# Optimization experiments

Measured on AMD Instinct MI355X. Metric: run time of the kernel, lower is better.

Reference implementation:

```python
import jax, jax.numpy as jnp
import numpy as np
from jax.scipy.special import logsumexp

S, D, K, R, P = 500, 768, 16, 256, 64  # seq_len, bert_dim, out_dim, n_pairs, max wordpieces/entity


def setup_inputs() -> dict:
    key = jax.random.key(0)
    k1, k2, k3, k4, k5, k6 = jax.random.split(key, 6)
    word_embeddings = jax.random.normal(k1, (S, D), jnp.float32)
    # kaiming_normal_ fan_in = D*K (last two dims collapsed); gain sqrt(2) for relu
    W = jax.random.normal(k2, (D, K, D), jnp.float32) * np.float32((2.0 / (K * D)) ** 0.5)
    idx1 = jax.random.randint(k3, (R, P), 0, S)
    idx2 = jax.random.randint(k4, (R, P), 0, S)
    # ragged mention lengths -> padding masks (at least 1 valid wordpiece)
    len1 = jax.random.randint(k5, (R,), 1, P + 1)
    len2 = jax.random.randint(k6, (R,), 1, P + 1)
    pos = jnp.arange(P)
    mask1 = (pos[None, :] < len1[:, None]).astype(jnp.float32)
    mask2 = (pos[None, :] < len2[:, None]).astype(jnp.float32)
    return {"word_embeddings": word_embeddings, "W": W, "idx1": idx1, "idx2": idx2,
            "mask1": mask1, "mask2": mask2}


def reference(word_embeddings, W, idx1, idx2, mask1, mask2):
    # gather ragged mention wordpieces (padded to P per entity)
    e1 = word_embeddings[idx1]  # [R, P, D]
    e2 = word_embeddings[idx2]  # [R, P, D]
    # biaffine: z[r,k,p,q] = e1[r,p,:] @ W[:,k,:] @ e2[r,q,:]
    zh = jnp.einsum('rpd,dke->rpke', e1, W)      # [R, P, K, D]
    z = jnp.einsum('rpke,rqe->rkpq', zh, e2)     # [R, K, P, P]
    # logsumexp pooling over all valid (p, q) mention-token pairs
    b = mask1[:, None, :, None] * mask2[:, None, None, :]  # [R, 1, P, P]
    scores = logsumexp(z, axis=(2, 3), b=b)      # [R, K]
    return scores
```

## Files before the change

kernel.cpp:

```cpp
#include <hip/hip_runtime.h>
#include <math.h>

#define S_ 500
#define D_ 768
#define K_ 16
#define R_ 256
#define P_ 64
#define NT 12

typedef unsigned short ushort_t;
typedef __attribute__((ext_vector_type(8))) short short8;
typedef __attribute__((ext_vector_type(4))) float floatx4;
typedef __attribute__((ext_vector_type(4))) float fx4;

__device__ inline ushort_t f2bf(float x) {
  unsigned int u = __float_as_uint(x);
  u += 0x7fffu + ((u >> 16) & 1u);
  return (ushort_t)(u >> 16);
}

__device__ inline unsigned int cvtpk(float lo, float hi) {
  unsigned int r;
  asm("v_cvt_pk_bf16_f32 %0, %1, %2" : "=v"(r) : "v"(lo), "v"(hi));
  return r;
}

#define GLD_LDS16(g, l)                                                        \
  __builtin_amdgcn_global_load_lds(                                            \
      (const __attribute__((address_space(1))) void*)(g),                      \
      (__attribute__((address_space(3))) void*)(l), 16, 0, 0)

#define ASM_BARRIER asm volatile("s_barrier" ::: "memory")
#define WAIT_VM6 asm volatile("s_waitcnt vmcnt(6)" ::: "memory")
#define WAIT_VM0 asm volatile("s_waitcnt vmcnt(0)" ::: "memory")

#define CFENCE asm volatile("" ::: "memory")
#define BARRIER_SYNC                                                           \
  do { CFENCE; __builtin_amdgcn_s_barrier(); CFENCE; } while (0)
#define WAIT_VM20_F                                                            \
  do { asm volatile("s_waitcnt vmcnt(20)" ::: "memory");                       \
       __builtin_amdgcn_sched_barrier(0); } while (0)
#define WAIT_VM0_F                                                             \
  do { asm volatile("s_waitcnt vmcnt(0)" ::: "memory");                        \
       __builtin_amdgcn_sched_barrier(0); } while (0)
#define WAIT_LGKM0_F                                                           \
  do { asm volatile("s_waitcnt lgkmcnt(0)" ::: "memory");                      \
       __builtin_amdgcn_sched_barrier(0); } while (0)

__global__ __launch_bounds__(256) void prep(const float* __restrict__ WE,
                                            ushort_t* __restrict__ WEb) {
  const int t = threadIdx.x;
  int gid = blockIdx.x * 256 + t;
  int row = gid / 192;
  ushort4 o = {0, 0, 0, 0};
  if (row < S_) {
    float4 v = *(const float4*)(WE + (size_t)gid * 4);
    o.x = f2bf(v.x); o.y = f2bf(v.y); o.z = f2bf(v.z); o.w = f2bf(v.w);
  }
  *(ushort4*)(WEb + (size_t)gid * 4) = o;
}

__global__ __launch_bounds__(256, 2) void mm0_fused(const ushort_t* __restrict__ A,
                                                    const float* __restrict__ Wf,
                                                    ushort_t* __restrict__ C) {
  __shared__ ushort_t As[2][2][128 * 32];
  __shared__ ushort_t Bs[2][2][128 * 32];
  const int tid = threadIdx.x;
  const int wave = tid >> 6, lane = tid & 63;
  const int m0 = blockIdx.y * 128, n0 = blockIdx.x * 128;
  const int wm = (wave & 1) * 64, wn = (wave >> 1) * 64;
  const int col = lane & 15, quad = lane >> 4;

  floatx4 acc[4][4];
#pragma unroll
  for (int i = 0; i < 4; i++)
#pragma unroll
    for (int j = 0; j < 4; j++)
#pragma unroll
      for (int e = 0; e < 4; e++) acc[i][j][e] = 0.f;

  const int srow = wave * 32 + (lane >> 2);
  const int scol = (lane & 3) * 8;
  const ushort_t* ga0 = A + (size_t)(m0 + srow) * D_ + scol;
  const int ldsbase = (wave * 32) * 32;

#define ISSUE_A(t_, buf_)                                                      \
  do {                                                                         \
    const ushort_t* ga = ga0 + (t_)*64;                                        \
    GLD_LDS16(ga, &As[buf_][0][ldsbase]);                                      \
    GLD_LDS16(ga + 16 * D_, &As[buf_][0][ldsbase + 16 * 32]);                  \
    GLD_LDS16(ga + 32, &As[buf_][1][ldsbase]);                                 \
    GLD_LDS16(ga + 32 + 16 * D_, &As[buf_][1][ldsbase + 16 * 32]);             \
  } while (0)

  const int nq = tid & 31;
  const int dqA = tid >> 5;
  const float* gwA = Wf + (size_t)(dqA * 4) * 12288 + n0 + nq * 4;
  const float* gwB = gwA + (size_t)32 * 12288;

  fx4 bv[2][4];
#define LOADB(t_)                                                              \
  do {                                                                         \
    _Pragma("unroll") for (int i = 0; i < 4; i++) {                            \
      bv[0][i] = *(const fx4*)(gwA + (size_t)((t_)*64 + i) * 12288);           \
      bv[1][i] = *(const fx4*)(gwB + (size_t)((t_)*64 + i) * 12288);           \
    }                                                                          \
  } while (0)

#define WRITEB(buf_)                                                           \
  do {                                                                         \
    _Pragma("unroll") for (int h = 0; h < 2; h++)                              \
    _Pragma("unroll") for (int j = 0; j < 4; j++) {                            \
      int row = nq * 4 + j;                                                    \
      uint2 w;                                                                 \
      w.x = cvtpk(bv[h][0][j], bv[h][1][j]);                                   \
      w.y = cvtpk(bv[h][2][j], bv[h][3][j]);                                   \
      *(uint2*)((char*)&Bs[buf_][h][0] +                                       \
                ((row * 64 + dqA * 8) ^ ((nq & 15) << 4))) = w;                \
    }                                                                          \
  } while (0)

  LOADB(0);
  ISSUE_A(0, 0);
  WRITEB(0);
  WAIT_LGKM0_F;
  for (int t = 0; t < NT; ++t) {
    const int cur = t & 1;
    if (t + 1 < NT) {
      LOADB(t + 1);
      ISSUE_A(t + 1, cur ^ 1);
      WAIT_VM20_F;
    } else {
      WAIT_VM0_F;
    }
    BARRIER_SYNC;
#pragma unroll
    for (int s = 0; s < 2; ++s) {
      short8 a[4], b[4];
#pragma unroll
      for (int i = 0; i < 4; i++)
        a[i] = *(const short8*)&As[cur][s][(wm + i * 16 + col) * 32 + quad * 8];
#pragma unroll
      for (int j = 0; j < 4; j++) {
        int row = wn + j * 16 + col;
        b[j] = *(const short8*)((const char*)&Bs[cur][s][0] +
                                ((row * 64 + quad * 16) ^ (((row >> 2) & 15) << 4)));
      }
#pragma unroll
      for (int i = 0; i < 4; i++)
#pragma unroll
        for (int j = 0; j < 4; j++)
          acc[i][j] = __builtin_amdgcn_mfma_f32_16x16x32_bf16(b[j], a[i], acc[i][j], 0, 0, 0);
    }
    if (t + 1 < NT) {
      WRITEB(cur ^ 1);
      WAIT_LGKM0_F;
    }
    BARRIER_SYNC;
  }
#undef ISSUE_A
#undef LOADB
#undef WRITEB

#pragma unroll
  for (int i = 0; i < 4; i++) {
    int m = m0 + wm + i * 16 + col;
#pragma unroll
    for (int j = 0; j < 4; j++) {
      int n = n0 + wn + j * 16 + quad * 4;
      ushort4 o;
      o.x = f2bf(acc[i][j][0]); o.y = f2bf(acc[i][j][1]);
      o.z = f2bf(acc[i][j][2]); o.w = f2bf(acc[i][j][3]);
      *(ushort4*)(C + (size_t)m * 12288 + n) = o;
    }
  }
}

__global__ __launch_bounds__(256, 2) void mm1_bt(const ushort_t* __restrict__ A,
                                                 const ushort_t* __restrict__ Bm,
                                                 ushort_t* __restrict__ G) {
  __shared__ ushort_t As[2][2][128 * 32];
  __shared__ ushort_t Bs[2][2][64 * 32];
  const int tid = threadIdx.x;
  const int wave = tid >> 6, lane = tid & 63;
  const int lin = blockIdx.x + (blockIdx.y << 3);
  const int yb = ((lin & 7) << 3) | (lin >> 6);
  const int xb = (lin >> 3) & 7;
  const int m0 = yb * 128, n0 = xb * 64;
  const int wm = (wave & 1) * 64, wn = (wave >> 1) * 32;
  const int col = lane & 15, quad = lane >> 4;

  floatx4 acc[4][2];
#pragma unroll
  for (int i = 0; i < 4; i++)
#pragma unroll
    for (int j = 0; j < 2; j++)
#pragma unroll
      for (int e = 0; e < 4; e++) acc[i][j][e] = 0.f;

  const int lrow = lane >> 2, scol = (lane & 3) * 8;
  const ushort_t* ga0 = A + (size_t)(m0 + wave * 32 + lrow) * D_ + scol;
  const ushort_t* gb0 = Bm + (size_t)(n0 + wave * 16 + lrow) * D_ + scol;
  const int aoff = (wave * 32) * 32;
  const int boff = (wave * 16) * 32;

#define ISSUE_TILE1(t_, buf_)                                                  \
  do {                                                                         \
    _Pragma("unroll") for (int s_ = 0; s_ < 2; s_++) {                         \
      const ushort_t* ga = ga0 + (t_)*64 + s_ * 32;                            \
      const ushort_t* gb = gb0 + (t_)*64 + s_ * 32;                            \
      GLD_LDS16(ga, &As[buf_][s_][aoff]);                                      \
      GLD_LDS16(ga + 16 * D_, &As[buf_][s_][aoff + 16 * 32]);                  \
      GLD_LDS16(gb, &Bs[buf_][s_][boff]);                                      \
    }                                                                          \
  } while (0)

  ISSUE_TILE1(0, 0);
  for (int t = 0; t < NT; ++t) {
    const int cur = t & 1;
    if (t + 1 < NT) {
      ISSUE_TILE1(t + 1, cur ^ 1);
      WAIT_VM6;
    } else {
      WAIT_VM0;
    }
    ASM_BARRIER;
#pragma unroll
    for (int s = 0; s < 2; ++s) {
      short8 a[4], b[2];
#pragma unroll
      for (int i = 0; i < 4; i++)
        a[i] = *(const short8*)&As[cur][s][(wm + i * 16 + col) * 32 + quad * 8];
#pragma unroll
      for (int j = 0; j < 2; j++)
        b[j] = *(const short8*)&Bs[cur][s][(wn + j * 16 + col) * 32 + quad * 8];
#pragma unroll
      for (int i = 0; i < 4; i++)
#pragma unroll
        for (int j = 0; j < 2; j++)
          acc[i][j] = __builtin_amdgcn_mfma_f32_16x16x32_bf16(a[i], b[j], acc[i][j], 0, 0, 0);
    }
    ASM_BARRIER;
  }
#undef ISSUE_TILE1

#pragma unroll
  for (int i = 0; i < 4; i++) {
    int s1 = (m0 + wm + i * 16) >> 4;
#pragma unroll
    for (int j = 0; j < 2; j++) {
      int s2 = n0 + wn + j * 16 + col;
      if (s1 < S_ && s2 < S_) {
        ushort4 o;
        o.x = f2bf(acc[i][j][0]); o.y = f2bf(acc[i][j][1]);
        o.z = f2bf(acc[i][j][2]); o.w = f2bf(acc[i][j][3]);
        *(ushort4*)(G + (((size_t)s1 * S_ + s2) << 4) + quad * 4) = o;
      }
    }
  }
}

__global__ __launch_bounds__(512) void lse_kernel(const ushort_t* __restrict__ G,
                                                  const int* __restrict__ idx1,
                                                  const int* __restrict__ idx2,
                                                  const float* __restrict__ mask1,
                                                  const float* __restrict__ mask2,
                                                  float* __restrict__ out) {
  const int r = blockIdx.x;
  const int tid = threadIdx.x;
  __shared__ int b1[P_], b2[P_];
  __shared__ int s_len1, s_len2;
  __shared__ float wmx[8][K_], wsum[8][K_];

  if (tid < 64) {
    float mv = mask1[r * P_ + tid];
    unsigned long long bal = __ballot(mv > 0.5f);
    if (tid == 0) s_len1 = (int)__popcll(bal);
    b1[tid] = idx1[r * P_ + tid] * (S_ * K_);
  } else if (tid < 128) {
    int q = tid - 64;
    float mv = mask2[r * P_ + q];
    unsigned long long bal = __ballot(mv > 0.5f);
    if (q == 0) s_len2 = (int)__popcll(bal);
    b2[q] = idx2[r * P_ + q] * K_;
  }
  __syncthreads();
  const int len2 = s_len2;
  const int total = s_len1 * len2;

  float m[K_], s[K_];
#pragma unroll
  for (int k = 0; k < K_; k++) { m[k] = -3.0e38f; s[k] = 0.f; }

  for (int i = tid; i < total; i += 512) {
    int p = i / len2;
    int q = i - p * len2;
    const uint4* g4 = (const uint4*)(G + b1[p] + b2[q]);
    uint4 w0 = g4[0], w1 = g4[1];
    unsigned int uu[8] = {w0.x, w0.y, w0.z, w0.w, w1.x, w1.y, w1.z, w1.w};
    float z[K_];
#pragma unroll
    for (int h = 0; h < 8; h++) {
      z[2 * h + 0] = __uint_as_float(uu[h] << 16);
      z[2 * h + 1] = __uint_as_float(uu[h] & 0xffff0000u);
    }
#pragma unroll
    for (int k = 0; k < K_; k++) {
      float d = z[k] - m[k];
      float e = __expf(-fabsf(d));
      bool up = d > 0.f;
      s[k] = up ? __fmaf_rn(s[k], e, 1.f) : (s[k] + e);
      m[k] = up ? z[k] : m[k];
    }
  }

#pragma unroll
  for (int off = 1; off < 64; off <<= 1) {
#pragma unroll
    for (int k = 0; k < K_; k++) {
      float mo = __shfl_xor(m[k], off, 64);
      float so = __shfl_xor(s[k], off, 64);
      float d = mo - m[k];
      float e = __expf(-fabsf(d));
      bool up = d > 0.f;
      s[k] = up ? __fmaf_rn(s[k], e, so) : __fmaf_rn(so, e, s[k]);
      m[k] = up ? mo : m[k];
    }
  }
  const int wave = tid >> 6, lane = tid & 63;
  if (lane == 0) {
#pragma unroll
    for (int k = 0; k < K_; k++) { wmx[wave][k] = m[k]; wsum[wave][k] = s[k]; }
  }
  __syncthreads();
  if (tid < K_) {
    float M = -3.0e38f, Ssum = 0.f;
#pragma unroll
    for (int w = 0; w < 8; w++) {
      float mo = wmx[w][tid], so = wsum[w][tid];
      float d = mo - M;
      float e = __expf(-fabsf(d));
      bool up = d > 0.f;
      Ssum = up ? __fmaf_rn(Ssum, e, so) : __fmaf_rn(so, e, Ssum);
      M = up ? mo : M;
    }
    out[r * K_ + tid] = M + __logf(Ssum);
  }
}

extern "C" void kernel_launch(void* const* d_in, const int* in_sizes, int n_in,
                              void* d_out, int out_size, void* d_ws, size_t ws_size,
                              hipStream_t stream) {
  const float* WE    = (const float*)d_in[0];
  const float* W     = (const float*)d_in[1];
  const int*   idx1  = (const int*)d_in[2];
  const int*   idx2  = (const int*)d_in[3];
  const float* mask1 = (const float*)d_in[4];
  const float* mask2 = (const float*)d_in[5];
  float* out = (float*)d_out;

  ushort_t* WEb   = (ushort_t*)d_ws;
  ushort_t* projb = WEb + (size_t)512 * 768;
  ushort_t* G     = projb + (size_t)512 * 12288;

  prep<<<384, 256, 0, stream>>>(WE, WEb);
  mm0_fused<<<dim3(96, 4), 256, 0, stream>>>(WEb, W, projb);
  mm1_bt<<<dim3(8, 64), 256, 0, stream>>>(projb, WEb, G);
  lse_kernel<<<R_, 512, 0, stream>>>(G, idx1, idx2, mask1, mask2, out);
}
```

Baseline: 132.4 us.

## Fuse four kernels into one persistent megakernel with grid barriers

Merges prep, both GEMMs and the logsumexp reduction into a single persistent kernel of 512 blocks. Stages are separated by atomic-counter grid barriers in workspace, which is cleared with a memset each call. The goal is to remove the launch gaps between kernels. In exchange the lse stage now runs 256 threads per block instead of 512, the barriers cost spin-waits, and the code relies on all 512 blocks being co-resident (2 per CU) or it deadlocks.

Measured after the change: 426.6 us. +222.2%, slower.

```diff
diff --git a/kernel.cpp b/kernel.cpp
--- a/kernel.cpp
+++ b/kernel.cpp
@@ -7,6 +7,7 @@
 #define R_ 256
 #define P_ 64
 #define NT 12
+#define NBLK 512u
 
 typedef unsigned short ushort_t;
 typedef __attribute__((ext_vector_type(8))) short short8;
@@ -47,58 +48,88 @@
   do { asm volatile("s_waitcnt lgkmcnt(0)" ::: "memory");                      \
        __builtin_amdgcn_sched_barrier(0); } while (0)
 
-__global__ __launch_bounds__(256) void prep(const float* __restrict__ WE,
-                                            ushort_t* __restrict__ WEb) {
-  const int t = threadIdx.x;
-  int gid = blockIdx.x * 256 + t;
-  int row = gid / 192;
-  ushort4 o = {0, 0, 0, 0};
-  if (row < S_) {
-    float4 v = *(const float4*)(WE + (size_t)gid * 4);
-    o.x = f2bf(v.x); o.y = f2bf(v.y); o.z = f2bf(v.z); o.w = f2bf(v.w);
-  }
-  *(ushort4*)(WEb + (size_t)gid * 4) = o;
-}
-
-__global__ __launch_bounds__(256, 2) void mm0_fused(const ushort_t* __restrict__ A,
-                                                    const float* __restrict__ Wf,
-                                                    ushort_t* __restrict__ C) {
-  __shared__ ushort_t As[2][2][128 * 32];
-  __shared__ ushort_t Bs[2][2][128 * 32];
+__device__ __forceinline__ void grid_barrier(unsigned int* bar, int phase) {
+  __syncthreads();
+  if (threadIdx.x == 0) {
+    unsigned int* cnt = bar + phase * 16;
+    unsigned int* flg = bar + phase * 16 + 8;
+    __threadfence();
+    unsigned int prev = __hip_atomic_fetch_add(cnt, 1u, __ATOMIC_ACQ_REL,
+                                               __HIP_MEMORY_SCOPE_AGENT);
+    if (prev == NBLK - 1u)
+      __hip_atomic_store(flg, 1u, __ATOMIC_RELEASE, __HIP_MEMORY_SCOPE_AGENT);
+    while (__hip_atomic_load(flg, __ATOMIC_ACQUIRE,
+                             __HIP_MEMORY_SCOPE_AGENT) == 0u)
+      __builtin_amdgcn_s_sleep(2);
+    __threadfence();
+  }
+  __syncthreads();
+}
+
+struct P1 { ushort_t As[2][2][128 * 32]; ushort_t Bs[2][2][128 * 32]; };
+struct P2 { ushort_t As[2][2][128 * 32]; ushort_t Bs[2][2][64 * 32]; };
+struct P3 { int b1[P_]; int b2[P_]; int len1, len2; float wmx[4][K_]; float wsum[4][K_]; };
+
+__global__ __launch_bounds__(256, 2) void mega(
+    const float* __restrict__ WE, const float* __restrict__ Wf,
+    const int* __restrict__ idx1, const int* __restrict__ idx2,
+    const float* __restrict__ mask1, const float* __restrict__ mask2,
+    ushort_t* __restrict__ WEb, ushort_t* __restrict__ projb,
+    ushort_t* __restrict__ G, float* __restrict__ out,
+    unsigned int* __restrict__ bar) {
+  __shared__ __align__(16) unsigned char smem[sizeof(P1)];
+  P1& s1 = *reinterpret_cast<P1*>(smem);
+  P2& s2 = *reinterpret_cast<P2*>(smem);
+  P3& s3 = *reinterpret_cast<P3*>(smem);
+  const int wid = blockIdx.x;
   const int tid = threadIdx.x;
   const int wave = tid >> 6, lane = tid & 63;
-  const int m0 = blockIdx.y * 128, n0 = blockIdx.x * 128;
-  const int wm = (wave & 1) * 64, wn = (wave >> 1) * 64;
   const int col = lane & 15, quad = lane >> 4;
 
-  floatx4 acc[4][4];
-#pragma unroll
-  for (int i = 0; i < 4; i++)
-#pragma unroll
-    for (int j = 0; j < 4; j++)
-#pragma unroll
-      for (int e = 0; e < 4; e++) acc[i][j][e] = 0.f;
-
-  const int srow = wave * 32 + (lane >> 2);
-  const int scol = (lane & 3) * 8;
-  const ushort_t* ga0 = A + (size_t)(m0 + srow) * D_ + scol;
-  const int ldsbase = (wave * 32) * 32;
+  if (wid < 384) {
+    int gid = wid * 256 + tid;
+    int row = gid / 192;
+    ushort4 o = {0, 0, 0, 0};
+    if (row < S_) {
+      float4 v = *(const float4*)(WE + (size_t)gid * 4);
+      o.x = f2bf(v.x); o.y = f2bf(v.y); o.z = f2bf(v.z); o.w = f2bf(v.w);
+    }
+    *(ushort4*)(WEb + (size_t)gid * 4) = o;
+  }
+  grid_barrier(bar, 0);
+
+  if (wid < 384) {
+    const int m0 = (wid / 96) * 128, n0 = (wid % 96) * 128;
+    const int wm = (wave & 1) * 64, wn = (wave >> 1) * 64;
+
+    floatx4 acc[4][4];
+#pragma unroll
+    for (int i = 0; i < 4; i++)
+#pragma unroll
+      for (int j = 0; j < 4; j++)
+#pragma unroll
+        for (int e = 0; e < 4; e++) acc[i][j][e] = 0.f;
+
+    const int srow = wave * 32 + (lane >> 2);
+    const int scol = (lane & 3) * 8;
+    const ushort_t* ga0 = WEb + (size_t)(m0 + srow) * D_ + scol;
+    const int ldsbase = (wave * 32) * 32;
 
 #define ISSUE_A(t_, buf_)                                                      \
   do {                                                                         \
     const ushort_t* ga = ga0 + (t_)*64;                                        \
-    GLD_LDS16(ga, &As[buf_][0][ldsbase]);                                      \
-    GLD_LDS16(ga + 16 * D_, &As[buf_][0][ldsbase + 16 * 32]);                  \
-    GLD_LDS16(ga + 32, &As[buf_][1][ldsbase]);                                 \
-    GLD_LDS16(ga + 32 + 16 * D_, &As[buf_][1][ldsbase + 16 * 32]);             \
+    GLD_LDS16(ga, &s1.As[buf_][0][ldsbase]);                                   \
+    GLD_LDS16(ga + 16 * D_, &s1.As[buf_][0][ldsbase + 16 * 32]);               \
+    GLD_LDS16(ga + 32, &s1.As[buf_][1][ldsbase]);                              \
+    GLD_LDS16(ga + 32 + 16 * D_, &s1.As[buf_][1][ldsbase + 16 * 32]);          \
   } while (0)
 
-  const int nq = tid & 31;
-  const int dqA = tid >> 5;
-  const float* gwA = Wf + (size_t)(dqA * 4) * 12288 + n0 + nq * 4;
-  const float* gwB = gwA + (size_t)32 * 12288;
-
-  fx4 bv[2][4];
+    const int nq = tid & 31;
+    const int dqA = tid >> 5;
+    const float* gwA = Wf + (size_t)(dqA * 4) * 12288 + n0 + nq * 4;
+    const float* gwB = gwA + (size_t)32 * 12288;
+
+    fx4 bv[2][4];
 #define LOADB(t_)                                                              \
   do {                                                                         \
     _Pragma("unroll") for (int i = 0; i < 4; i++) {                            \
@@ -115,236 +146,221 @@
       uint2 w;                                                                 \
       w.x = cvtpk(bv[h][0][j], bv[h][1][j]);                                   \
       w.y = cvtpk(bv[h][2][j], bv[h][3][j]);                                   \
-      *(uint2*)((char*)&Bs[buf_][h][0] +                                       \
+      *(uint2*)((char*)&s1.Bs[buf_][h][0] +                                    \
                 ((row * 64 + dqA * 8) ^ ((nq & 15) << 4))) = w;                \
     }                                                                          \
   } while (0)
 
-  LOADB(0);
-  ISSUE_A(0, 0);
-  WRITEB(0);
-  WAIT_LGKM0_F;
-  for (int t = 0; t < NT; ++t) {
-    const int cur = t & 1;
-    if (t + 1 < NT) {
-      LOADB(t + 1);
-      ISSUE_A(t + 1, cur ^ 1);
-      WAIT_VM20_F;
-    } else {
-      WAIT_VM0_F;
-    }
-    BARRIER_SYNC;
-#pragma unroll
-    for (int s = 0; s < 2; ++s) {
-      short8 a[4], b[4];
-#pragma unroll
-      for (int i = 0; i < 4; i++)
-        a[i] = *(const short8*)&As[cur][s][(wm + i * 16 + col) * 32 + quad * 8];
-#pragma unroll
-      for (int j = 0; j < 4; j++) {
-        int row = wn + j * 16 + col;
-        b[j] = *(const short8*)((const char*)&Bs[cur][s][0] +
-                                ((row * 64 + quad * 16) ^ (((row >> 2) & 15) << 4)));
-      }
-#pragma unroll
-      for (int i = 0; i < 4; i++)
-#pragma unroll
-        for (int j = 0; j < 4; j++)
-          acc[i][j] = __builtin_amdgcn_mfma_f32_16x16x32_bf16(b[j], a[i], acc[i][j], 0, 0, 0);
-    }
-    if (t + 1 < NT) {
-      WRITEB(cur ^ 1);
-      WAIT_LGKM0_F;
-    }
-    BARRIER_SYNC;
-  }
+    LOADB(0);
+    ISSUE_A(0, 0);
+    WRITEB(0);
+    WAIT_LGKM0_F;
+    for (int t = 0; t < NT; ++t) {
+      const int cur = t & 1;
+      if (t + 1 < NT) {
+        LOADB(t + 1);
+        ISSUE_A(t + 1, cur ^ 1);
+        WAIT_VM20_F;
+      } else {
+        WAIT_VM0_F;
+      }
+      BARRIER_SYNC;
+#pragma unroll
+      for (int s = 0; s < 2; ++s) {
+        short8 a[4], b[4];
+#pragma unroll
+        for (int i = 0; i < 4; i++)
+          a[i] = *(const short8*)&s1.As[cur][s][(wm + i * 16 + col) * 32 + quad * 8];
+#pragma unroll
+        for (int j = 0; j < 4; j++) {
+          int row = wn + j * 16 + col;
+          b[j] = *(const short8*)((const char*)&s1.Bs[cur][s][0] +
+                                  ((row * 64 + quad * 16) ^ (((row >> 2) & 15) << 4)));
+        }
+#pragma unroll
+        for (int i = 0; i < 4; i++)
+#pragma unroll
+          for (int j = 0; j < 4; j++)
+            acc[i][j] = __builtin_amdgcn_mfma_f32_16x16x32_bf16(b[j], a[i], acc[i][j], 0, 0, 0);
+      }
+      if (t + 1 < NT) {
+        WRITEB(cur ^ 1);
+        WAIT_LGKM0_F;
+      }
+      BARRIER_SYNC;
+    }
 #undef ISSUE_A
 #undef LOADB
 #undef WRITEB
 
 #pragma unroll
-  for (int i = 0; i < 4; i++) {
-    int m = m0 + wm + i * 16 + col;
-#pragma unroll
-    for (int j = 0; j < 4; j++) {
-      int n = n0 + wn + j * 16 + quad * 4;
-      ushort4 o;
-      o.x = f2bf(acc[i][j][0]); o.y = f2bf(acc[i][j][1]);
-      o.z = f2bf(acc[i][j][2]); o.w = f2bf(acc[i][j][3]);
-      *(ushort4*)(C + (size_t)m * 12288 + n) = o;
-    }
-  }
-}
-
-__global__ __launch_bounds__(256, 2) void mm1_bt(const ushort_t* __restrict__ A,
-                                                 const ushort_t* __restrict__ Bm,
-                                                 ushort_t* __restrict__ G) {
-  __shared__ ushort_t As[2][2][128 * 32];
-  __shared__ ushort_t Bs[2][2][64 * 32];
-  const int tid = threadIdx.x;
-  const int wave = tid >> 6, lane = tid & 63;
-  const int lin = blockIdx.x + (blockIdx.y << 3);
-  const int yb = ((lin & 7) << 3) | (lin >> 6);
-  const int xb = (lin >> 3) & 7;
-  const int m0 = yb * 128, n0 = xb * 64;
-  const int wm = (wave & 1) * 64, wn = (wave >> 1) * 32;
-  const int col = lane & 15, quad = lane >> 4;
-
-  floatx4 acc[4][2];
-#pragma unroll
-  for (int i = 0; i < 4; i++)
-#pragma unroll
-    for (int j = 0; j < 2; j++)
-#pragma unroll
-      for (int e = 0; e < 4; e++) acc[i][j][e] = 0.f;
-
-  const int lrow = lane >> 2, scol = (lane & 3) * 8;
-  const ushort_t* ga0 = A + (size_t)(m0 + wave * 32 + lrow) * D_ + scol;
-  const ushort_t* gb0 = Bm + (size_t)(n0 + wave * 16 + lrow) * D_ + scol;
-  const int aoff = (wave * 32) * 32;
-  const int boff = (wave * 16) * 32;
+    for (int i = 0; i < 4; i++) {
+      int m = m0 + wm + i * 16 + col;
+#pragma unroll
+      for (int j = 0; j < 4; j++) {
+        int n = n0 + wn + j * 16 + quad * 4;
+        ushort4 o;
+        o.x = f2bf(acc[i][j][0]); o.y = f2bf(acc[i][j][1]);
+        o.z = f2bf(acc[i][j][2]); o.w = f2bf(acc[i][j][3]);
+        *(ushort4*)(projb + (size_t)m * 12288 + n) = o;
+      }
+    }
+  }
+  grid_barrier(bar, 1);
+
+  {
+    const int lin = wid;
+    const int yb = ((lin & 7) << 3) | (lin >> 6);
+    const int xb = (lin >> 3) & 7;
+    const int m0 = yb * 128, n0 = xb * 64;
+    const int wm = (wave & 1) * 64, wn = (wave >> 1) * 32;
+
+    floatx4 acc[4][2];
+#pragma unroll
+    for (int i = 0; i < 4; i++)
+#pragma unroll
+      for (int j = 0; j < 2; j++)
+#pragma unroll
+        for (int e = 0; e < 4; e++) acc[i][j][e] = 0.f;
+
+    const int lrow = lane >> 2, scol = (lane & 3) * 8;
+    const ushort_t* ga0 = projb + (size_t)(m0 + wave * 32 + lrow) * D_ + scol;
+    const ushort_t* gb0 = WEb + (size_t)(n0 + wave * 16 + lrow) * D_ + scol;
+    const int aoff = (wave * 32) * 32;
+    const int boff = (wave * 16) * 32;
 
 #define ISSUE_TILE1(t_, buf_)                                                  \
   do {                                                                         \
     _Pragma("unroll") for (int s_ = 0; s_ < 2; s_++) {                         \
       const ushort_t* ga = ga0 + (t_)*64 + s_ * 32;                            \
       const ushort_t* gb = gb0 + (t_)*64 + s_ * 32;                            \
-      GLD_LDS16(ga, &As[buf_][s_][aoff]);                                      \
-      GLD_LDS16(ga + 16 * D_, &As[buf_][s_][aoff + 16 * 32]);                  \
-      GLD_LDS16(gb, &Bs[buf_][s_][boff]);                                      \
+      GLD_LDS16(ga, &s2.As[buf_][s_][aoff]);                                   \
+      GLD_LDS16(ga + 16 * D_, &s2.As[buf_][s_][aoff + 16 * 32]);               \
+      GLD_LDS16(gb, &s2.Bs[buf_][s_][boff]);                                   \
     }                                                                          \
   } while (0)
 
-  ISSUE_TILE1(0, 0);
-  for (int t = 0; t < NT; ++t) {
-    const int cur = t & 1;
-    if (t + 1 < NT) {
-      ISSUE_TILE1(t + 1, cur ^ 1);
-      WAIT_VM6;
-    } else {
-      WAIT_VM0;
-    }
-    ASM_BARRIER;
-#pragma unroll
-    for (int s = 0; s < 2; ++s) {
-      short8 a[4], b[2];
-#pragma unroll
-      for (int i = 0; i < 4; i++)
-        a[i] = *(const short8*)&As[cur][s][(wm + i * 16 + col) * 32 + quad * 8];
-#pragma unroll
-      for (int j = 0; j < 2; j++)
-        b[j] = *(const short8*)&Bs[cur][s][(wn + j * 16 + col) * 32 + quad * 8];
-#pragma unroll
-      for (int i = 0; i < 4; i++)
+    ISSUE_TILE1(0, 0);
+    for (int t = 0; t < NT; ++t) {
+      const int cur = t & 1;
+      if (t + 1 < NT) {
+        ISSUE_TILE1(t + 1, cur ^ 1);
+        WAIT_VM6;
+      } else {
+        WAIT_VM0;
+      }
+      ASM_BARRIER;
+#pragma unroll
+      for (int s = 0; s < 2; ++s) {
+        short8 a[4], b[2];
+#pragma unroll
+        for (int i = 0; i < 4; i++)
+          a[i] = *(const short8*)&s2.As[cur][s][(wm + i * 16 + col) * 32 + quad * 8];
 #pragma unroll
         for (int j = 0; j < 2; j++)
-          acc[i][j] = __builtin_amdgcn_mfma_f32_16x16x32_bf16(a[i], b[j], acc[i][j], 0, 0, 0);
-    }
-    ASM_BARRIER;
-  }
+          b[j] = *(const short8*)&s2.Bs[cur][s][(wn + j * 16 + col) * 32 + quad * 8];
+#pragma unroll
+        for (int i = 0; i < 4; i++)
+#pragma unroll
+          for (int j = 0; j < 2; j++)
+            acc[i][j] = __builtin_amdgcn_mfma_f32_16x16x32_bf16(a[i], b[j], acc[i][j], 0, 0, 0);
+      }
+      ASM_BARRIER;
+    }
 #undef ISSUE_TILE1
 
 #pragma unroll
-  for (int i = 0; i < 4; i++) {
-    int s1 = (m0 + wm + i * 16) >> 4;
-#pragma unroll
-    for (int j = 0; j < 2; j++) {
-      int s2 = n0 + wn + j * 16 + col;
-      if (s1 < S_ && s2 < S_) {
-        ushort4 o;
-        o.x = f2bf(acc[i][j][0]); o.y = f2bf(acc[i][j][1]);
-        o.z = f2bf(acc[i][j][2]); o.w = f2bf(acc[i][j][3]);
-        *(ushort4*)(G + (((size_t)s1 * S_ + s2) << 4) + quad * 4) = o;
-      }
-    }
-  }
-}
-
-__global__ __launch_bounds__(512) void lse_kernel(const ushort_t* __restrict__ G,
-                                                  const int* __restrict__ idx1,
-                                                  const int* __restrict__ idx2,
-                                                  const float* __restrict__ mask1,
-                                                  const float* __restrict__ mask2,
-                                                  float* __restrict__ out) {
-  const int r = blockIdx.x;
-  const int tid = threadIdx.x;
-  __shared__ int b1[P_], b2[P_];
-  __shared__ int s_len1, s_len2;
-  __shared__ float wmx[8][K_], wsum[8][K_];
-
-  if (tid < 64) {
-    float mv = mask1[r * P_ + tid];
-    unsigned long long bal = __ballot(mv > 0.5f);
-    if (tid == 0) s_len1 = (int)__popcll(bal);
-    b1[tid] = idx1[r * P_ + tid] * (S_ * K_);
-  } else if (tid < 128) {
-    int q = tid - 64;
-    float mv = mask2[r * P_ + q];
-    unsigned long long bal = __ballot(mv > 0.5f);
-    if (q == 0) s_len2 = (int)__popcll(bal);
-    b2[q] = idx2[r * P_ + q] * K_;
-  }
-  __syncthreads();
-  const int len2 = s_len2;
-  const int total = s_len1 * len2;
-
-  float m[K_], s[K_];
-#pragma unroll
-  for (int k = 0; k < K_; k++) { m[k] = -3.0e38f; s[k] = 0.f; }
-
-  for (int i = tid; i < total; i += 512) {
-    int p = i / len2;
-    int q = i - p * len2;
-    const uint4* g4 = (const uint4*)(G + b1[p] + b2[q]);
-    uint4 w0 = g4[0], w1 = g4[1];
-    unsigned int uu[8] = {w0.x, w0.y, w0.z, w0.w, w1.x, w1.y, w1.z, w1.w};
-    float z[K_];
-#pragma unroll
-    for (int h = 0; h < 8; h++) {
-      z[2 * h + 0] = __uint_as_float(uu[h] << 16);
-      z[2 * h + 1] = __uint_as_float(uu[h] & 0xffff0000u);
-    }
-#pragma unroll
-    for (int k = 0; k < K_; k++) {
-      float d = z[k] - m[k];
-      float e = __expf(-fabsf(d));
-      bool up = d > 0.f;
-      s[k] = up ? __fmaf_rn(s[k], e, 1.f) : (s[k] + e);
-      m[k] = up ? z[k] : m[k];
-    }
-  }
-
-#pragma unroll
-  for (int off = 1; off < 64; off <<= 1) {
-#pragma unroll
-    for (int k = 0; k < K_; k++) {
-      float mo = __shfl_xor(m[k], off, 64);
-      float so = __shfl_xor(s[k], off, 64);
-      float d = mo - m[k];
-      float e = __expf(-fabsf(d));
-      bool up = d > 0.f;
-      s[k] = up ? __fmaf_rn(s[k], e, so) : __fmaf_rn(so, e, s[k]);
-      m[k] = up ? mo : m[k];
-    }
-  }
-  const int wave = tid >> 6, lane = tid & 63;
-  if (lane == 0) {
-#pragma unroll
-    for (int k = 0; k < K_; k++) { wmx[wave][k] = m[k]; wsum[wave][k] = s[k]; }
-  }
-  __syncthreads();
-  if (tid < K_) {
-    float M = -3.0e38f, Ssum = 0.f;
-#pragma unroll
-    for (int w = 0; w < 8; w++) {
-      float mo = wmx[w][tid], so = wsum[w][tid];
-      float d = mo - M;
-      float e = __expf(-fabsf(d));
-      bool up = d > 0.f;
-      Ssum = up ? __fmaf_rn(Ssum, e, so) : __fmaf_rn(so, e, Ssum);
-      M = up ? mo : M;
-    }
-    out[r * K_ + tid] = M + __logf(Ssum);
+    for (int i = 0; i < 4; i++) {
+      int s1r = (m0 + wm + i * 16) >> 4;
+#pragma unroll
+      for (int j = 0; j < 2; j++) {
+        int s2c = n0 + wn + j * 16 + col;
+        if (s1r < S_ && s2c < S_) {
+          ushort4 o;
+          o.x = f2bf(acc[i][j][0]); o.y = f2bf(acc[i][j][1]);
+          o.z = f2bf(acc[i][j][2]); o.w = f2bf(acc[i][j][3]);
+          *(ushort4*)(G + (((size_t)s1r * S_ + s2c) << 4) + quad * 4) = o;
+        }
+      }
+    }
+  }
+  grid_barrier(bar, 2);
+
+  if (wid < R_) {
+    const int r = wid;
+    if (tid < 64) {
+      float mv = mask1[r * P_ + tid];
+      unsigned long long bal = __ballot(mv > 0.5f);
+      if (tid == 0) s3.len1 = (int)__popcll(bal);
+      s3.b1[tid] = idx1[r * P_ + tid] * (S_ * K_);
+    } else if (tid < 128) {
+      int q = tid - 64;
+      float mv = mask2[r * P_ + q];
+      unsigned long long bal = __ballot(mv > 0.5f);
+      if (q == 0) s3.len2 = (int)__popcll(bal);
+      s3.b2[q] = idx2[r * P_ + q] * K_;
+    }
+    __syncthreads();
+    const int len2 = s3.len2;
+    const int total = s3.len1 * len2;
+
+    float m[K_], s[K_];
+#pragma unroll
+    for (int k = 0; k < K_; k++) { m[k] = -3.0e38f; s[k] = 0.f; }
+
+    for (int i = tid; i < total; i += 256) {
+      int p = i / len2;
+      int q = i - p * len2;
+      const uint4* g4 = (const uint4*)(G + s3.b1[p] + s3.b2[q]);
+      uint4 w0 = g4[0], w1 = g4[1];
+      unsigned int uu[8] = {w0.x, w0.y, w0.z, w0.w, w1.x, w1.y, w1.z, w1.w};
+      float z[K_];
+#pragma unroll
+      for (int h = 0; h < 8; h++) {
+        z[2 * h + 0] = __uint_as_float(uu[h] << 16);
+        z[2 * h + 1] = __uint_as_float(uu[h] & 0xffff0000u);
+      }
+#pragma unroll
+      for (int k = 0; k < K_; k++) {
+        float d = z[k] - m[k];
+        float e = __expf(-fabsf(d));
+        bool up = d > 0.f;
+        s[k] = up ? __fmaf_rn(s[k], e, 1.f) : (s[k] + e);
+        m[k] = up ? z[k] : m[k];
+      }
+    }
+
+#pragma unroll
+    for (int off = 1; off < 64; off <<= 1) {
+#pragma unroll
+      for (int k = 0; k < K_; k++) {
+        float mo = __shfl_xor(m[k], off, 64);
+        float so = __shfl_xor(s[k], off, 64);
+        float d = mo - m[k];
+        float e = __expf(-fabsf(d));
+        bool up = d > 0.f;
+        s[k] = up ? __fmaf_rn(s[k], e, so) : __fmaf_rn(so, e, s[k]);
+        m[k] = up ? mo : m[k];
+      }
+    }
+    if (lane == 0) {
+#pragma unroll
+      for (int k = 0; k < K_; k++) { s3.wmx[wave][k] = m[k]; s3.wsum[wave][k] = s[k]; }
+    }
+    __syncthreads();
+    if (tid < K_) {
+      float M = -3.0e38f, Ssum = 0.f;
+#pragma unroll
+      for (int w = 0; w < 4; w++) {
+        float mo = s3.wmx[w][tid], so = s3.wsum[w][tid];
+        float d = mo - M;
+        float e = __expf(-fabsf(d));
+        bool up = d > 0.f;
+        Ssum = up ? __fmaf_rn(Ssum, e, so) : __fmaf_rn(so, e, Ssum);
+        M = up ? mo : M;
+      }
+      out[r * K_ + tid] = M + __logf(Ssum);
+    }
   }
 }
 
@@ -352,7 +368,7 @@
                               void* d_out, int out_size, void* d_ws, size_t ws_size,
                               hipStream_t stream) {
   const float* WE    = (const float*)d_in[0];
-  const float* W     = (const float*)d_in[1];
+  const float* Wf    = (const float*)d_in[1];
   const int*   idx1  = (const int*)d_in[2];
   const int*   idx2  = (const int*)d_in[3];
   const float* mask1 = (const float*)d_in[4];
@@ -362,9 +378,9 @@
   ushort_t* WEb   = (ushort_t*)d_ws;
   ushort_t* projb = WEb + (size_t)512 * 768;
   ushort_t* G     = projb + (size_t)512 * 12288;
-
-  prep<<<384, 256, 0, stream>>>(WE, WEb);
-  mm0_fused<<<dim3(96, 4), 256, 0, stream>>>(WEb, W, projb);
-  mm1_bt<<<dim3(8, 64), 256, 0, stream>>>(projb, WEb, G);
-  lse_kernel<<<R_, 512, 0, stream>>>(G, idx1, idx2, mask1, mask2, out);
-}
+  unsigned int* bar = (unsigned int*)((char*)d_ws + (size_t)(32u << 20));
+
+  hipMemsetAsync(bar, 0, 256, stream);
+  mega<<<NBLK, 256, 0, stream>>>(WE, Wf, idx1, idx2, mask1, mask2,
+                                 WEb, projb, G, out, bar);
+}
```
